# Performance work log

Hardware: AMD Instinct MI355X
Metric: run time of the kernel (lower is better)

The kernel has to match this reference:

```python
import jax, jax.numpy as jnp
import numpy as np

H = W = 1024          # image_shape (square)
ZP, PH, PW = 16, 32, 32   # psf z-stack shape
THRESH = 2.0          # detection_threshold
K = 1024              # spots_per_frame
ROISIZE = PW          # default roisize = psf.shape[-1]
BG_R = PW * 2         # default bg_filter_size
MAXF = PW             # default max_filter_size


def setup_inputs() -> dict:
    key = jax.random.key(0)
    k1, k2 = jax.random.split(key)
    image = jax.random.uniform(k1, (H, W), jnp.float32) * 100.0
    psf = jax.random.uniform(k2, (ZP, PH, PW), jnp.float32)
    psf = psf / jnp.sum(psf, axis=(1, 2), keepdims=True)  # normalized PSF stack
    return {"image": image, "psf": psf}


def _precompute_filters(psf):
    pad = (H - PH) // 2  # square image/psf -> same pad both dims
    psf_padded = jnp.pad(psf, ((0, 0), (pad, pad), (pad, pad)))
    psf_padded = jnp.fft.fftshift(psf_padded, axes=(1, 2))
    psf_fd = jnp.flip(jnp.fft.fft2(psf_padded), axis=(1, 2))
    rr = (jnp.arange(H) - H // 2)[:, None] ** 2 + (jnp.arange(W) - W // 2)[None, :] ** 2
    bg = (rr < BG_R ** 2).astype(jnp.float32) / (np.pi * BG_R ** 2)
    bg_fd = jnp.fft.fft2(jnp.fft.fftshift(bg))
    return psf_fd, bg_fd


def reference(image, psf):
    psf_fd, bg_fd = _precompute_filters(psf)
    image_fd = jnp.fft.fft2(image)
    conv_psf = jnp.fft.ifft2(image_fd[None] * psf_fd).real       # [Z,H,W]
    conv_bg = jnp.fft.ifft2(image_fd * bg_fd).real               # [H,W]
    ratio = conv_psf / (conv_bg[None] + 1.0)                     # matched-filter SNR
    result = ratio.max(axis=0)                                   # [H,W]
    zmap = jnp.argmax(ratio, axis=0)                             # best z plane

    # MaxPool2d(MAXF, stride=1, padding=MAXF//2-1): torch pads with -inf,
    # output is [H-1,W-1]; torch code then zero-pads one row/col at top-left.
    p = MAXF // 2 - 1
    mx = jax.lax.reduce_window(result, -jnp.inf, jax.lax.max,
                               (MAXF, MAXF), (1, 1), ((p, p), (p, p)))
    mx = jnp.pad(mx, ((1, 0), (1, 0)))                           # back to [H,W]

    mask = jnp.where((mx == result) & (result > THRESH), result, 0.0)
    values, indices = jax.lax.top_k(mask.ravel(), K)
    x = indices % W
    y = indices // H  # torch divides by input_shape[0]; square so == W
    roy = y - ROISIZE // 2
    rox = x - ROISIZE // 2
    valid = ((values > THRESH)
             & (roy >= 0) & (roy < H - ROISIZE)
             & (rox >= 0) & (rox < W - ROISIZE))

    # fixed-shape version of boolean select: clamp for safe gather, mask invalids
    roy_c = jnp.clip(roy, 0, H - ROISIZE)
    rox_c = jnp.clip(rox, 0, W - ROISIZE)
    r = jnp.arange(ROISIZE)
    Y = roy_c[:, None, None] + r[None, :, None]                  # [K,R,1]
    X = rox_c[:, None, None] + r[None, None, :]                  # [K,1,R]
    rois = image[Y, X] * valid[:, None, None].astype(image.dtype)  # [K,R,R]

    roipos = jnp.stack((roy_c, rox_c), -1) * valid[:, None]
    intensity = values * valid
    return roipos, intensity, rois, valid
```

## Files before the change

### kernel.cpp

```cpp
#include <hip/hip_runtime.h>
#include <stdint.h>

typedef float v4f __attribute__((ext_vector_type(4)));

#define PEX_STRIDE 1156
#define CSTRIDE 858
#define WS_IMG8   0
#define WS_BFRAG  1048576
#define WS_PEX    1064960
#define WS_RESULT 9994240
#define WS_CAND   14188544

__device__ inline unsigned char f32_to_e4m3(float v) {
    if (!(v > 0.0f)) return 0;
    if (v >= 448.0f) return 0x7e;
    if (v < 0.015625f) {
        int m = (int)(v * 512.0f + 0.5f);
        if (m > 7) return 0x08;
        return (unsigned char)m;
    }
    unsigned int u = __float_as_uint(v) + 0x00080000u;
    int e = (int)((u >> 23) & 0xff) - 127;
    int m3 = (int)(u >> 20) & 7;
    int e8 = e + 7;
    if (e8 >= 16) return 0x7e;
    return (unsigned char)((e8 << 3) | m3);
}

__global__ void k_pex(const float* __restrict__ img, float* __restrict__ pex,
                      uint32_t* __restrict__ img8, const float* __restrict__ psf,
                      unsigned char* __restrict__ bf, unsigned int* cnt,
                      float4* __restrict__ out, int n4) {
    __shared__ float wtot[4];
    int blk = blockIdx.x, t = threadIdx.x;
    if (blk >= 1024) {
        if (blk < 2080) {
            int i = (blk - 1024) * 256 + t;
            if (i < n4) { float4 z; z.x = z.y = z.z = z.w = 0.f; out[i] = z; }
        } else {
            int u = (blk - 2080) * 256 + t;
            if (u == 0) cnt[0] = 0u;
            int kb = u >> 9; int l = (u >> 3) & 63; int j = u & 7;
            int z = l & 15; int q = l >> 4;
            int a = kb; int b = q * 8 + j;
            float p = psf[z * 1024 + a * 32 + b];
            float c = cosf((float)(a + b - 32) * (6.283185307179586f / 1024.0f));
            bf[kb * 512 + l * 8 + j] = f32_to_e4m3(p * c * 1024.0f);
        }
        return;
    }
    int r = blk;
    const float* row = img + r * 1024;
    float s[5];
    float acc = 0.f;
    int base = t * 5;
    #pragma unroll
    for (int j = 0; j < 5; j++) {
        int c = base + j;
        float v = (c < 1152) ? row[(c - 64) & 1023] : 0.f;
        acc += v; s[j] = acc;
    }
    float sc = acc;
    int lane = t & 63, w = t >> 6;
    #pragma unroll
    for (int off = 1; off < 64; off <<= 1) {
        float v = __shfl_up(sc, off, 64);
        if (lane >= off) sc += v;
    }
    if (lane == 63) wtot[w] = sc;
    __syncthreads();
    float wbase = 0.f;
    #pragma unroll
    for (int i = 0; i < 3; i++) if (i < w) wbase += wtot[i];
    float excl = wbase + (sc - acc);
    float* prow = pex + r * PEX_STRIDE;
    if (t == 0) prow[0] = 0.f;
    #pragma unroll
    for (int j = 0; j < 5; j++) {
        int c = base + j;
        if (c < 1152) prow[c + 1] = excl + s[j];
    }
    float4 v4 = *(const float4*)(row + 4 * t);
    img8[r * 256 + t] = (uint32_t)f32_to_e4m3(v4.x)
                      | ((uint32_t)f32_to_e4m3(v4.y) << 8)
                      | ((uint32_t)f32_to_e4m3(v4.z) << 16)
                      | ((uint32_t)f32_to_e4m3(v4.w) << 24);
}

__global__ __launch_bounds__(512, 4) void k_conv(
    const unsigned long long* __restrict__ img64,
    const unsigned long long* __restrict__ bfrag,
    const float* __restrict__ pex, float* __restrict__ result) {
    __shared__ unsigned long long sm[8 * CSTRIDE];
    __shared__ float rbp[8][5][8];
    __shared__ float rbv[8][5];
    int tid = threadIdx.x;
    int wave = tid >> 6, lane = tid & 63;
    int b = blockIdx.x;
    int tr = b >> 5, tc = b & 31;
    int r0 = tr * 64, c0 = tc * 32;

    for (int u = tid; u < 665; u += 512) {
        int dr = u / 7;
        int x8 = u - dr * 7;
        int row = (r0 + dr - 16) & 1023;
        int cb0 = (c0 + x8 * 8 - 16) & 1023;
        int cb1 = (cb0 + 8) & 1023;
        unsigned long long lo = img64[row * 128 + (cb0 >> 3)];
        unsigned long long hi = img64[row * 128 + (cb1 >> 3)];
        int dst = dr * 9 + x8;
        sm[dst] = lo;
        #pragma unroll
        for (int s = 1; s < 8; s++)
            sm[s * CSTRIDE + dst] = (lo >> (8 * s)) | (hi << (64 - 8 * s));
    }

    if (lane < 40) {
        int si = lane / 5, kc = lane - si * 5;
        int baserow = r0 + si * 8 + 3;
        int n = c0 + 8 * kc;
        int j0 = wave * 16;
        int j1 = j0 + 16; if (j1 > 127) j1 = 127;
        float acc = 0.f;
        for (int j = j0; j < j1; j++) {
            int dy = j - 63;
            int ady = dy < 0 ? -dy : dy;
            int w = (int)sqrtf((float)(4095 - ady * ady));
            const float* p = pex + ((baserow + dy) & 1023) * PEX_STRIDE + n;
            acc += p[65 + w] - p[64 - w];
        }
        rbp[si][kc][wave] = acc;
    }
    __syncthreads();
    if (tid < 40) {
        int si = tid / 5, kc = tid - si * 5;
        float s = 0.f;
        #pragma unroll
        for (int h = 0; h < 8; h++) s += rbp[si][kc][h];
        const float kk = (float)(1.0 / (3.14159265358979323846 * 4096.0));
        rbv[si][kc] = 1.0f / ((s * kk + 1.0f) * 1024.0f);
    }

    int i0 = (wave >> 1) * 16;
    int cw = (wave & 1) * 16;
    int g = lane >> 4;
    int slot = ((cw + (lane & 15)) >> 3) + g;
    const unsigned long long* bp = sm + (lane & 7) * CSTRIDE + slot + i0 * 9;

    v4f acc[16];
    #pragma unroll
    for (int f = 0; f < 16; f++) acc[f] = (v4f)0.0f;

    unsigned long long bwin[16];
    #pragma unroll
    for (int s = 0; s < 16; s++) bwin[s] = bp[s * 9];

    unsigned long long anext = bfrag[lane];
    for (int kbo = 0; kbo < 32; kbo += 16) {
        #pragma unroll
        for (int kk = 0; kk < 16; kk++) {
            int kb = kbo + kk;
            unsigned long long acur = anext;
            anext = bfrag[((kb < 31 ? kb + 1 : 31) << 6) + lane];
            unsigned long long nb = bp[(kb < 31 ? kb + 16 : 46) * 9];
            #pragma unroll
            for (int cc = 0; cc < 16; cc++) {
                acc[cc] = __builtin_amdgcn_mfma_f32_16x16x32_fp8_fp8(
                    (long)acur, (long)bwin[(kk + cc) & 15], acc[cc], 0, 0, 0);
            }
            bwin[kk & 15] = nb;
        }
    }
    __syncthreads();

    float zmax[16];
    #pragma unroll
    for (int cc = 0; cc < 16; cc++) {
        v4f v = acc[cc];
        float m = fmaxf(fmaxf(v.x, v.y), fmaxf(v.z, v.w));
        m = fmaxf(m, __shfl_xor(m, 16, 64));
        m = fmaxf(m, __shfl_xor(m, 32, 64));
        zmax[cc] = m;
    }
    int u = cw + (lane & 15);
    int kc = u >> 3;
    float fr = (float)(u & 7) * 0.125f;
    int gcol = c0 + u;
    #pragma unroll
    for (int c4 = 0; c4 < 4; c4++) {
        float m01 = (g & 1) ? zmax[c4 * 4 + 1] : zmax[c4 * 4 + 0];
        float m23 = (g & 1) ? zmax[c4 * 4 + 3] : zmax[c4 * 4 + 2];
        float m = (g & 2) ? m23 : m01;
        int lrow = i0 + c4 * 4 + g;
        int sil = lrow >> 3;
        float rv0 = rbv[sil][kc], rv1 = rbv[sil][kc + 1];
        float rbl = rv0 + fr * (rv1 - rv0);
        result[(r0 + lrow) * 1024 + gcol] = m * rbl;
    }
}

__global__ __launch_bounds__(256) void k_maxcand(const float* __restrict__ result,
                                                 unsigned int* cnt,
                                                 unsigned long long* cand) {
    __shared__ float ls[95 * 96];
    __shared__ float hr[95 * 64];
    __shared__ float wmax[4];
    int bx = blockIdx.x & 15, by = blockIdx.x >> 4;
    int i0 = by * 64, j0 = bx * 64;
    int t = threadIdx.x;
    const float4* cb4 = (const float4*)(result + i0 * 1024 + j0);
    float mx = -3.4e38f;
    #pragma unroll
    for (int k = 0; k < 4; k++) {
        int idx = k * 256 + t;
        float4 v = cb4[(idx >> 4) * 256 + (idx & 15)];
        mx = fmaxf(mx, fmaxf(fmaxf(v.x, v.y), fmaxf(v.z, v.w)));
    }
    #pragma unroll
    for (int m = 1; m < 64; m <<= 1) mx = fmaxf(mx, __shfl_xor(mx, m, 64));
    if ((t & 63) == 0) wmax[t >> 6] = mx;
    __syncthreads();
    float tmax = fmaxf(fmaxf(wmax[0], wmax[1]), fmaxf(wmax[2], wmax[3]));
    if (tmax <= 2.0f) return;

    for (int idx = t; idx < 95 * 95; idx += 256) {
        int r = idx / 95, c = idx - r * 95;
        int gr = i0 - 16 + r, gc = j0 - 16 + c;
        float v = -3.4e38f;
        if ((unsigned)gr < 1024u && (unsigned)gc < 1024u) v = result[gr * 1024 + gc];
        ls[r * 96 + c] = v;
    }
    __syncthreads();
    for (int idx = t; idx < 95 * 64; idx += 256) {
        int r = idx >> 6, c = idx & 63;
        const float* p = ls + r * 96 + c;
        float m = p[0];
        #pragma unroll
        for (int d = 1; d < 32; d++) m = fmaxf(m, p[d]);
        hr[idx] = m;
    }
    __syncthreads();
    for (int idx = t; idx < 64 * 64; idx += 256) {
        int r = idx >> 6, c = idx & 63;
        const float* p = hr + r * 64 + c;
        float m = p[0];
        #pragma unroll
        for (int d = 1; d < 32; d++) m = fmaxf(m, p[d * 64]);
        float v = ls[(r + 16) * 96 + (c + 16)];
        int gi = i0 + r, gj = j0 + c;
        if (gi >= 1 && gj >= 1 && v > 2.0f && v == m) {
            unsigned int k = atomicAdd(cnt, 1u);
            if (k < 2048)
                cand[k] = ((unsigned long long)__float_as_uint(v) << 32)
                        | (unsigned int)(~(unsigned int)(gi * 1024 + gj));
        }
    }
}

__global__ __launch_bounds__(1024) void k_final(
    const float* __restrict__ image, const unsigned int* __restrict__ cnt,
    const unsigned long long* __restrict__ cand, float* __restrict__ out) {
    __shared__ unsigned long long keys[2048];
    int t = threadIdx.x;
    int n = (int)cnt[0]; if (n > 2048) n = 2048;
    if (n == 0) return;
    for (int k = t; k < 2048; k += 1024) keys[k] = (k < n) ? cand[k] : 0ull;
    __syncthreads();
    for (int size = 2; size <= 2048; size <<= 1) {
        for (int stride = size >> 1; stride > 0; stride >>= 1) {
            for (int i = t; i < 2048; i += 1024) {
                int ixj = i ^ stride;
                if (ixj > i) {
                    unsigned long long a = keys[i], b = keys[ixj];
                    bool sw = ((i & size) == 0) ? (a < b) : (a > b);
                    if (sw) { keys[i] = b; keys[ixj] = a; }
                }
            }
            __syncthreads();
        }
    }
    float* roipos = out;
    float* intensity = out + 2048;
    float* rois = out + 3072;
    float* validf = out + 3072 + 1048576;
    int nw = n < 1024 ? n : 1024;
    if (t < nw) {
        unsigned long long key = keys[t];
        float val = __uint_as_float((unsigned int)(key >> 32));
        unsigned int p = ~(unsigned int)key;
        int y = (int)(p >> 10), x = (int)(p & 1023);
        int roy = y - 16, rox = x - 16;
        bool valid = (roy >= 0 && roy < 992 && rox >= 0 && rox < 992);
        int royc = roy < 0 ? 0 : (roy > 992 ? 992 : roy);
        int roxc = rox < 0 ? 0 : (rox > 992 ? 992 : rox);
        roipos[2 * t]     = valid ? (float)royc : 0.f;
        roipos[2 * t + 1] = valid ? (float)roxc : 0.f;
        intensity[t]      = valid ? val : 0.f;
        validf[t]         = valid ? 1.f : 0.f;
    }
    __syncthreads();
    for (int k = 0; k < nw; k++) {
        unsigned long long key = keys[k];
        unsigned int p = ~(unsigned int)key;
        int y = (int)(p >> 10), x = (int)(p & 1023);
        int roy = y - 16, rox = x - 16;
        if (!(roy >= 0 && roy < 992 && rox >= 0 && rox < 992)) continue;
        int u = t >> 5, vv = t & 31;
        rois[k * 1024 + t] = image[(roy + u) * 1024 + (rox + vv)];
    }
}

extern "C" void kernel_launch(void* const* d_in, const int* in_sizes, int n_in,
                              void* d_out, int out_size, void* d_ws, size_t ws_size,
                              hipStream_t stream) {
    const float* image = (const float*)d_in[0];
    const float* psf   = (const float*)d_in[1];
    float* out = (float*)d_out;
    char* ws = (char*)d_ws;
    unsigned char* img8  = (unsigned char*)(ws + WS_IMG8);
    unsigned char* bfrag = (unsigned char*)(ws + WS_BFRAG);
    float* pex = (float*)(ws + WS_PEX);
    float* result = (float*)(ws + WS_RESULT);
    unsigned int* cnt = (unsigned int*)(ws + WS_CAND);
    unsigned long long* cand = (unsigned long long*)(ws + WS_CAND + 16);

    int n4 = out_size / 4;
    hipLaunchKernelGGL(k_pex,     dim3(2144), dim3(256), 0, stream,
                       image, pex, (uint32_t*)img8, psf, bfrag, cnt, (float4*)d_out, n4);
    hipLaunchKernelGGL(k_conv,    dim3(512),  dim3(512), 0, stream,
                       (const unsigned long long*)img8, (const unsigned long long*)bfrag, pex, result);
    hipLaunchKernelGGL(k_maxcand, dim3(256),  dim3(256), 0, stream, result, cnt, cand);
    hipLaunchKernelGGL(k_final,   dim3(1),    dim3(1024), 0, stream, image, cnt, cand, out);
}
```

Before: 96.00 us.

## Switch conv MFMA from 16x16x32 fp8 to scaled 16x16x128 f8f6f4

Reorders the PSF fragment buffer into 32-byte per-lane chunks so the conv kernel can issue the gfx950 scaled MFMA 16x16x128 with neutral scales instead of the 16x16x32 fp8 MFMA. This cuts the MFMA instruction count by four. The loop is restructured from 16 live accumulators with a sliding B window into two accumulators per output pair, with B fragments loaded from LDS as 4x64-bit reads. Register pressure drops, but LDS reads are repeated across row tiles, and the k-reduction layout must match the new fragment order exactly.

```diff
diff --git a/kernel.cpp b/kernel.cpp
--- a/kernel.cpp
+++ b/kernel.cpp
@@ -2,6 +2,7 @@
 #include <stdint.h>
 
 typedef float v4f __attribute__((ext_vector_type(4)));
+typedef int   v8i __attribute__((ext_vector_type(8)));
 
 #define PEX_STRIDE 1156
 #define CSTRIDE 858
@@ -40,12 +41,11 @@
         } else {
             int u = (blk - 2080) * 256 + t;
             if (u == 0) cnt[0] = 0u;
-            int kb = u >> 9; int l = (u >> 3) & 63; int j = u & 7;
-            int z = l & 15; int q = l >> 4;
-            int a = kb; int b = q * 8 + j;
+            int kb4 = u >> 11; int l = (u >> 5) & 63; int b = u & 31;
+            int z = l & 15; int a = kb4 * 4 + (l >> 4);
             float p = psf[z * 1024 + a * 32 + b];
             float c = cosf((float)(a + b - 32) * (6.283185307179586f / 1024.0f));
-            bf[kb * 512 + l * 8 + j] = f32_to_e4m3(p * c * 1024.0f);
+            bf[u] = f32_to_e4m3(p * c * 1024.0f);
         }
         return;
     }
@@ -87,9 +87,15 @@
                       | ((uint32_t)f32_to_e4m3(v4.w) << 24);
 }
 
+__device__ inline v8i ldsB(const unsigned long long* p) {
+    union { unsigned long long q[4]; v8i v; } u;
+    u.q[0] = p[0]; u.q[1] = p[1]; u.q[2] = p[2]; u.q[3] = p[3];
+    return u.v;
+}
+
 __global__ __launch_bounds__(512, 4) void k_conv(
     const unsigned long long* __restrict__ img64,
-    const unsigned long long* __restrict__ bfrag,
+    const unsigned char* __restrict__ bfrag,
     const float* __restrict__ pex, float* __restrict__ result) {
     __shared__ unsigned long long sm[8 * CSTRIDE];
     __shared__ float rbp[8][5][8];
@@ -143,55 +149,52 @@
 
     int i0 = (wave >> 1) * 16;
     int cw = (wave & 1) * 16;
-    int g = lane >> 4;
-    int slot = ((cw + (lane & 15)) >> 3) + g;
-    const unsigned long long* bp = sm + (lane & 7) * CSTRIDE + slot + i0 * 9;
-
-    v4f acc[16];
-    #pragma unroll
-    for (int f = 0; f < 16; f++) acc[f] = (v4f)0.0f;
-
-    unsigned long long bwin[16];
-    #pragma unroll
-    for (int s = 0; s < 16; s++) bwin[s] = bp[s * 9];
-
-    unsigned long long anext = bfrag[lane];
-    for (int kbo = 0; kbo < 32; kbo += 16) {
-        #pragma unroll
-        for (int kk = 0; kk < 16; kk++) {
-            int kb = kbo + kk;
-            unsigned long long acur = anext;
-            anext = bfrag[((kb < 31 ? kb + 1 : 31) << 6) + lane];
-            unsigned long long nb = bp[(kb < 31 ? kb + 16 : 46) * 9];
+    int q = lane >> 4;
+    int n = lane & 15;
+    const unsigned long long* bpq =
+        sm + (n & 7) * CSTRIDE + ((cw + n) >> 3) + (i0 + q) * 9;
+    const v8i* bfA = (const v8i*)(bfrag + lane * 32);
+
+    float zmax[16];
+    #pragma unroll
+    for (int h = 0; h < 2; h++) {
+        #pragma unroll
+        for (int p = 0; p < 4; p++) {
+            const unsigned long long* tp = bpq + (h * 8 + p) * 9;
+            v4f a0 = (v4f)0.0f, a1 = (v4f)0.0f;
+            v8i bcur = ldsB(tp);
             #pragma unroll
-            for (int cc = 0; cc < 16; cc++) {
-                acc[cc] = __builtin_amdgcn_mfma_f32_16x16x32_fp8_fp8(
-                    (long)acur, (long)bwin[(kk + cc) & 15], acc[cc], 0, 0, 0);
+            for (int kb4 = 0; kb4 < 8; kb4++) {
+                v8i bnxt = ldsB(tp + (4 * (kb4 + 1)) * 9);
+                v8i av = bfA[kb4 << 6];
+                a0 = __builtin_amdgcn_mfma_scale_f32_16x16x128_f8f6f4(
+                        av, bcur, a0, 0, 0, 0, 0x7f7f7f7f, 0, 0x7f7f7f7f);
+                a1 = __builtin_amdgcn_mfma_scale_f32_16x16x128_f8f6f4(
+                        av, bnxt, a1, 0, 0, 0, 0x7f7f7f7f, 0, 0x7f7f7f7f);
+                bcur = bnxt;
             }
-            bwin[kk & 15] = nb;
-        }
-    }
-    __syncthreads();
-
-    float zmax[16];
-    #pragma unroll
-    for (int cc = 0; cc < 16; cc++) {
-        v4f v = acc[cc];
-        float m = fmaxf(fmaxf(v.x, v.y), fmaxf(v.z, v.w));
-        m = fmaxf(m, __shfl_xor(m, 16, 64));
-        m = fmaxf(m, __shfl_xor(m, 32, 64));
-        zmax[cc] = m;
-    }
-    int u = cw + (lane & 15);
-    int kc = u >> 3;
-    float fr = (float)(u & 7) * 0.125f;
-    int gcol = c0 + u;
+            float m0 = fmaxf(fmaxf(a0.x, a0.y), fmaxf(a0.z, a0.w));
+            m0 = fmaxf(m0, __shfl_xor(m0, 16, 64));
+            m0 = fmaxf(m0, __shfl_xor(m0, 32, 64));
+            zmax[h * 8 + p] = m0;
+            float m1 = fmaxf(fmaxf(a1.x, a1.y), fmaxf(a1.z, a1.w));
+            m1 = fmaxf(m1, __shfl_xor(m1, 16, 64));
+            m1 = fmaxf(m1, __shfl_xor(m1, 32, 64));
+            zmax[h * 8 + p + 4] = m1;
+        }
+    }
+    __syncthreads();
+
+    int uu = cw + n;
+    int kc = uu >> 3;
+    float fr = (float)(uu & 7) * 0.125f;
+    int gcol = c0 + uu;
     #pragma unroll
     for (int c4 = 0; c4 < 4; c4++) {
-        float m01 = (g & 1) ? zmax[c4 * 4 + 1] : zmax[c4 * 4 + 0];
-        float m23 = (g & 1) ? zmax[c4 * 4 + 3] : zmax[c4 * 4 + 2];
-        float m = (g & 2) ? m23 : m01;
-        int lrow = i0 + c4 * 4 + g;
+        float m01 = (q & 1) ? zmax[c4 * 4 + 1] : zmax[c4 * 4 + 0];
+        float m23 = (q & 1) ? zmax[c4 * 4 + 3] : zmax[c4 * 4 + 2];
+        float m = (q & 2) ? m23 : m01;
+        int lrow = i0 + c4 * 4 + q;
         int sil = lrow >> 3;
         float rv0 = rbv[sil][kc], rv1 = rbv[sil][kc + 1];
         float rbl = rv0 + fr * (rv1 - rv0);
@@ -328,7 +331,7 @@
     hipLaunchKernelGGL(k_pex,     dim3(2144), dim3(256), 0, stream,
                        image, pex, (uint32_t*)img8, psf, bfrag, cnt, (float4*)d_out, n4);
     hipLaunchKernelGGL(k_conv,    dim3(512),  dim3(512), 0, stream,
-                       (const unsigned long long*)img8, (const unsigned long long*)bfrag, pex, result);
+                       (const unsigned long long*)img8, bfrag, pex, result);
     hipLaunchKernelGGL(k_maxcand, dim3(256),  dim3(256), 0, stream, result, cnt, cand);
     hipLaunchKernelGGL(k_final,   dim3(1),    dim3(1024), 0, stream, image, cnt, cand, out);
 }
```

Result: slower. 293.8 us (+206.1%).
